# Kernel optimization log

Hardware: AMD Instinct MI355X
Metric: run time of the kernel (lower is better)

The kernel has to match this reference:

```python
import jax, jax.numpy as jnp
import numpy as np
from jax import lax

B, S, H = 2, 2048, 768
FF = 1536
E = 8
TOP_K = 2


def setup_inputs() -> dict:
    key = jax.random.key(0)
    k1, k2, k3, k4 = jax.random.split(key, 4)
    hidden_states = jax.random.normal(k1, (B, S, H), dtype=jnp.float32)
    # torch init: weight.normal_() for experts; nn.Linear default init for gate (approx normal here is fine for a numerics baseline)
    gate_w = jax.random.normal(k2, (E, H), dtype=jnp.float32) * 0.02
    w_fc = jax.random.normal(k3, (E, FF, H), dtype=jnp.float32) * 0.02
    w_proj = jax.random.normal(k4, (E, H, FF), dtype=jnp.float32) * 0.02
    return {"hidden_states": hidden_states, "gate_w": gate_w, "w_fc": w_fc, "w_proj": w_proj}


def reference(hidden_states, gate_w, w_fc, w_proj):
    b, s, h = hidden_states.shape
    x = hidden_states.reshape(-1, h)                      # [T, H]
    # --- top-k gating (logits in float32, as in the torch code) ---
    logits = (x @ gate_w.T).astype(jnp.float32)           # [T, E]
    top_logits, top_idx = lax.top_k(logits, TOP_K)        # [T, K]
    gates = jax.nn.softmax(top_logits, axis=1).astype(x.dtype)  # [T, K]
    # combined per-token/per-expert gate: g[t,e] = sum_k gates[t,k]*[idx[t,k]==e]
    onehot = jax.nn.one_hot(top_idx, E, dtype=x.dtype)    # [T, K, E]
    g = jnp.einsum('tk,tke->te', gates, onehot)           # [T, E]
    # --- experts: gather + per-expert GEMM + gated scatter-add combine ---
    # Equivalent math: tokens with zero gate for expert e contribute nothing,
    # so compute each expert on all tokens and weight by g[:, e].
    out = jnp.zeros_like(x)
    for e in range(E):  # fixed small loop over experts (structurally distinct weights)
        hmid = jax.nn.gelu(x @ w_fc[e].T, approximate=False)   # [T, FF] (torch gelu = erf form)
        out = out + g[:, e:e + 1] * (hmid @ w_proj[e].T)       # [T, H]
    out = out.reshape(b, s, h)
    return out, logits
```

## Files before the change

kernel.cpp:

```cpp
#include <hip/hip_runtime.h>
#include <hip/hip_bf16.h>
#include <math.h>
#include <stdint.h>

#define TOKENS 4096
#define HDIM   768
#define FFDIM  1536
#define NEXP   8

typedef __attribute__((ext_vector_type(8))) short bf16x8;
typedef __attribute__((ext_vector_type(4))) float f32x4;

__device__ __forceinline__ unsigned short f2bf(float f) {
    union { float f; uint32_t u; } c; c.f = f;
    uint32_t u = c.u;
    uint32_t r = (u + 0x7FFFu + ((u >> 16) & 1u)) >> 16;
    return (unsigned short)r;
}

__device__ __forceinline__ void gload_lds16(const void* g, void* l) {
    __builtin_amdgcn_global_load_lds(
        (const __attribute__((address_space(1))) void*)g,
        (__attribute__((address_space(3))) void*)l, 16, 0, 0);
}

__global__ void zero_init(float* __restrict__ outp, int n) {
    int i = blockIdx.x * blockDim.x + threadIdx.x;
    int stride = gridDim.x * blockDim.x;
    for (int j = i; j < n; j += stride) outp[j] = 0.f;
}

__global__ void cast_bf16(const float* __restrict__ src,
                          unsigned short* __restrict__ dst, int n4) {
    int stride = gridDim.x * blockDim.x;
    for (int i = blockIdx.x * blockDim.x + threadIdx.x; i < n4; i += stride) {
        float4 v = ((const float4*)src)[i];
        ushort4 o;
        o.x = f2bf(v.x); o.y = f2bf(v.y); o.z = f2bf(v.z); o.w = f2bf(v.w);
        ((ushort4*)dst)[i] = o;
    }
}

__global__ __launch_bounds__(256) void gating(
    const float* __restrict__ x, const float* __restrict__ gw,
    float* __restrict__ logits,
    int* __restrict__ tok_e, float* __restrict__ tok_g)
{
    int t = blockIdx.x * 4 + (threadIdx.x >> 6);
    int lane = threadIdx.x & 63;
    const float4* xt = (const float4*)(x + (size_t)t * HDIM);
    const float4* gw4 = (const float4*)gw;
    float acc[NEXP];
#pragma unroll
    for (int e = 0; e < NEXP; e++) acc[e] = 0.f;
#pragma unroll
    for (int it = 0; it < 3; it++) {
        int i = lane + it * 64;
        float4 xv = xt[i];
#pragma unroll
        for (int e = 0; e < NEXP; e++) {
            float4 wv = gw4[e * 192 + i];
            acc[e] += xv.x * wv.x + xv.y * wv.y + xv.z * wv.z + xv.w * wv.w;
        }
    }
#pragma unroll
    for (int e = 0; e < NEXP; e++) {
#pragma unroll
        for (int off = 32; off > 0; off >>= 1)
            acc[e] += __shfl_xor(acc[e], off);
    }
    if (lane == 0) {
        float4 l0 = make_float4(acc[0], acc[1], acc[2], acc[3]);
        float4 l1 = make_float4(acc[4], acc[5], acc[6], acc[7]);
        float4* lp = (float4*)(logits + (size_t)t * NEXP);
        lp[0] = l0; lp[1] = l1;
        int i0 = 0; float v0 = acc[0];
#pragma unroll
        for (int e = 1; e < NEXP; e++) if (acc[e] > v0) { v0 = acc[e]; i0 = e; }
        int i1 = -1; float v1 = -3.4e38f;
#pragma unroll
        for (int e = 0; e < NEXP; e++) if (e != i0 && acc[e] > v1) { v1 = acc[e]; i1 = e; }
        float g0 = 1.f / (1.f + expf(v1 - v0));
        tok_e[t * 2] = i0; tok_e[t * 2 + 1] = i1;
        tok_g[t * 2] = g0; tok_g[t * 2 + 1] = 1.f - g0;
    }
}

__global__ __launch_bounds__(1024) void build_lists(
    const int* __restrict__ tok_e, const float* __restrict__ tok_g,
    int* __restrict__ counts, int* __restrict__ entries,
    float* __restrict__ gates)
{
    __shared__ unsigned long long slo[1024], shi[1024];
    int tid = threadIdx.x;
    int eL[8]; float gL[8];
    int4 ea = ((const int4*)tok_e)[tid * 2];
    int4 eb = ((const int4*)tok_e)[tid * 2 + 1];
    float4 ga = ((const float4*)tok_g)[tid * 2];
    float4 gb = ((const float4*)tok_g)[tid * 2 + 1];
    eL[0] = ea.x; eL[1] = ea.y; eL[2] = ea.z; eL[3] = ea.w;
    eL[4] = eb.x; eL[5] = eb.y; eL[6] = eb.z; eL[7] = eb.w;
    gL[0] = ga.x; gL[1] = ga.y; gL[2] = ga.z; gL[3] = ga.w;
    gL[4] = gb.x; gL[5] = gb.y; gL[6] = gb.z; gL[7] = gb.w;

    unsigned long long clo = 0, chi = 0;
#pragma unroll
    for (int j = 0; j < 8; j++) {
        int e = eL[j];
        unsigned long long one = 1ull << ((e & 3) * 16);
        if (e < 4) clo += one; else chi += one;
    }
    slo[tid] = clo; shi[tid] = chi;
    __syncthreads();
    for (int s = 1; s < 1024; s <<= 1) {
        unsigned long long vlo = 0, vhi = 0;
        if (tid >= s) { vlo = slo[tid - s]; vhi = shi[tid - s]; }
        __syncthreads();
        slo[tid] += vlo; shi[tid] += vhi;
        __syncthreads();
    }
    unsigned long long rlo = slo[tid] - clo;
    unsigned long long rhi = shi[tid] - chi;
    if (tid == 0) {
        unsigned long long tlo = slo[1023], thi = shi[1023];
#pragma unroll
        for (int e = 0; e < 4; e++) {
            counts[e]     = (int)((tlo >> (e * 16)) & 0xFFFF);
            counts[e + 4] = (int)((thi >> (e * 16)) & 0xFFFF);
        }
    }
#pragma unroll
    for (int j = 0; j < 8; j++) {
        int e = eL[j];
        int sh = (e & 3) * 16;
        unsigned long long one = 1ull << sh;
        int slot;
        if (e < 4) { slot = (int)((rlo >> sh) & 0xFFFF); rlo += one; }
        else       { slot = (int)((rhi >> sh) & 0xFFFF); rhi += one; }
        entries[e * TOKENS + slot] = tid * 8 + j;
        gates[e * TOKENS + slot]   = gL[j];
    }
}

template<int KD, int ND, bool IS_FC>
__global__ __launch_bounds__(256) void moe_gemm(
    const unsigned short* __restrict__ Asrc,
    const unsigned short* __restrict__ Bsrc,
    const int* __restrict__ counts,
    const int* __restrict__ entries,
    const float* __restrict__ gates,
    unsigned short* __restrict__ hmid,
    float* __restrict__ outp)
{
    int e = blockIdx.z;
    int n_e = counts[e];
    int rowTile = blockIdx.y;
    if (rowTile * 64 >= n_e) return;
    int n0 = blockIdx.x * 64;

    __shared__ __align__(16) unsigned short sA[64 * 32];
    __shared__ __align__(16) unsigned short sB[64 * 32];

    int tid = threadIdx.x;
    int w = tid >> 6;
    int l = tid & 63;

    const int* lst = entries + e * TOKENS;

    int rL   = (w << 4) + (l >> 2);
    int p    = l & 3;
    int sseg = p ^ ((rL >> 1) & 3);

    int lrow = rowTile * 64 + rL;
    int idx  = lrow < n_e ? lrow : n_e - 1;
    int ent  = lst[idx];
    int arow = IS_FC ? (ent >> 1) : ent;

    const unsigned short* Ab = Asrc + (size_t)arow * KD + sseg * 8;
    const unsigned short* Bb = Bsrc + (size_t)e * ND * KD + (size_t)(n0 + rL) * KD + sseg * 8;
    unsigned short* sAw = sA + w * 512;
    unsigned short* sBw = sB + w * 512;

    int lo = l & 15;
    int q  = l >> 4;
    int pa = q ^ ((lo >> 1) & 3);
    int aOff     = w * 512 + lo * 32 + pa * 8;
    int bOffBase = lo * 32 + pa * 8;

    f32x4 acc[4];
#pragma unroll
    for (int i = 0; i < 4; i++) acc[i] = (f32x4){0.f, 0.f, 0.f, 0.f};

    for (int k0 = 0; k0 < KD; k0 += 32) {
        gload_lds16(Ab + k0, sAw);
        gload_lds16(Bb + k0, sBw);
        __syncthreads();
        bf16x8 va = *(const bf16x8*)(sA + aOff);
#pragma unroll
        for (int nt = 0; nt < 4; nt++) {
            bf16x8 vb = *(const bf16x8*)(sB + nt * 512 + bOffBase);
            acc[nt] = __builtin_amdgcn_mfma_f32_16x16x32_bf16(va, vb, acc[nt], 0, 0, 0);
        }
        __syncthreads();
    }

#pragma unroll
    for (int r = 0; r < 4; r++) {
        int orow = rowTile * 64 + (w << 4) + q * 4 + r;
        if (orow < n_e) {
            int oent = lst[orow];
            if (IS_FC) {
                size_t rowid = (size_t)oent;
#pragma unroll
                for (int nt = 0; nt < 4; nt++) {
                    float v = acc[nt][r];
                    v = 0.5f * v * (1.f + erff(v * 0.70710678118654752f));
                    hmid[rowid * FFDIM + n0 + nt * 16 + lo] = f2bf(v);
                }
            } else {
                int token = oent >> 1;
                float g = gates[e * TOKENS + orow];
#pragma unroll
                for (int nt = 0; nt < 4; nt++) {
                    atomicAdd(&outp[(size_t)token * HDIM + n0 + nt * 16 + lo],
                              acc[nt][r] * g);
                }
            }
        }
    }
}

extern "C" void kernel_launch(void* const* d_in, const int* in_sizes, int n_in,
                              void* d_out, int out_size, void* d_ws, size_t ws_size,
                              hipStream_t stream) {
    const float* x     = (const float*)d_in[0];
    const float* gw    = (const float*)d_in[1];
    const float* wfc   = (const float*)d_in[2];
    const float* wproj = (const float*)d_in[3];
    float* outp   = (float*)d_out;
    float* logits = outp + (size_t)TOKENS * HDIM;

    char* ws = (char*)d_ws;
    int*   counts  = (int*)ws;
    int*   entries = (int*)(ws + 256);
    float* gates   = (float*)(ws + 256 + NEXP * TOKENS * 4);
    size_t off = 256 + 2ull * NEXP * TOKENS * 4;
    int*   tok_e   = (int*)(ws + off);   off += (size_t)TOKENS * 2 * 4;
    float* tok_g   = (float*)(ws + off); off += (size_t)TOKENS * 2 * 4;
    unsigned short* x_bf   = (unsigned short*)(ws + off); off += (size_t)TOKENS * HDIM * 2;
    unsigned short* wfc_bf = (unsigned short*)(ws + off); off += (size_t)NEXP * FFDIM * HDIM * 2;
    unsigned short* wpj_bf = (unsigned short*)(ws + off); off += (size_t)NEXP * HDIM * FFDIM * 2;
    unsigned short* hmid   = (unsigned short*)(ws + off);

    zero_init<<<2048, 256, 0, stream>>>(outp, TOKENS * HDIM);
    cast_bf16<<<1536, 256, 0, stream>>>(x, x_bf, TOKENS * HDIM / 4);
    cast_bf16<<<2048, 256, 0, stream>>>(wfc, wfc_bf, NEXP * FFDIM * HDIM / 4);
    cast_bf16<<<2048, 256, 0, stream>>>(wproj, wpj_bf, NEXP * HDIM * FFDIM / 4);
    gating<<<TOKENS / 4, 256, 0, stream>>>(x, gw, logits, tok_e, tok_g);
    build_lists<<<1, 1024, 0, stream>>>(tok_e, tok_g, counts, entries, gates);
    moe_gemm<HDIM, FFDIM, true ><<<dim3(FFDIM / 64, 64, NEXP), 256, 0, stream>>>(
        x_bf, wfc_bf, counts, entries, gates, hmid, outp);
    moe_gemm<FFDIM, HDIM, false><<<dim3(HDIM / 64, 64, NEXP), 256, 0, stream>>>(
        hmid, wpj_bf, counts, entries, gates, hmid, outp);
}
```

Measured before the change: 264.8 us.

## Enlarge MoE GEMM tiles to 128x128, compact hmid layout, fuse x cast into gating

The MoE GEMM tile grows from 64x64 to 128x128, with each wave computing a 64x64 sub-tile of 4x4 MFMAs, so each loaded operand is reused more and LDS and global traffic per FLOP drops. hmid is now stored in expert-sorted compact rows (base offset plus slot) instead of indexed by entry, so the second GEMM reads its A rows contiguously. The separate x-to-bf16 cast kernel is folded into the gating kernel, removing one launch and one read of x. The trade-off is more accumulator registers per thread, lower occupancy, and fewer blocks in flight.

```diff
diff --git a/kernel.cpp b/kernel.cpp
--- a/kernel.cpp
+++ b/kernel.cpp
@@ -44,12 +44,14 @@
 __global__ __launch_bounds__(256) void gating(
     const float* __restrict__ x, const float* __restrict__ gw,
     float* __restrict__ logits,
-    int* __restrict__ tok_e, float* __restrict__ tok_g)
+    int* __restrict__ tok_e, float* __restrict__ tok_g,
+    unsigned short* __restrict__ x_bf)
 {
     int t = blockIdx.x * 4 + (threadIdx.x >> 6);
     int lane = threadIdx.x & 63;
     const float4* xt = (const float4*)(x + (size_t)t * HDIM);
     const float4* gw4 = (const float4*)gw;
+    ushort4* xbt = (ushort4*)(x_bf + (size_t)t * HDIM);
     float acc[NEXP];
 #pragma unroll
     for (int e = 0; e < NEXP; e++) acc[e] = 0.f;
@@ -57,6 +59,9 @@
     for (int it = 0; it < 3; it++) {
         int i = lane + it * 64;
         float4 xv = xt[i];
+        ushort4 o;
+        o.x = f2bf(xv.x); o.y = f2bf(xv.y); o.z = f2bf(xv.z); o.w = f2bf(xv.w);
+        xbt[i] = o;
 #pragma unroll
         for (int e = 0; e < NEXP; e++) {
             float4 wv = gw4[e * 192 + i];
@@ -88,8 +93,8 @@
 
 __global__ __launch_bounds__(1024) void build_lists(
     const int* __restrict__ tok_e, const float* __restrict__ tok_g,
-    int* __restrict__ counts, int* __restrict__ entries,
-    float* __restrict__ gates)
+    int* __restrict__ counts, int* __restrict__ bases,
+    int* __restrict__ entries, float* __restrict__ gates)
 {
     __shared__ unsigned long long slo[1024], shi[1024];
     int tid = threadIdx.x;
@@ -123,11 +128,15 @@
     unsigned long long rhi = shi[tid] - chi;
     if (tid == 0) {
         unsigned long long tlo = slo[1023], thi = shi[1023];
+        int c[8];
 #pragma unroll
         for (int e = 0; e < 4; e++) {
-            counts[e]     = (int)((tlo >> (e * 16)) & 0xFFFF);
-            counts[e + 4] = (int)((thi >> (e * 16)) & 0xFFFF);
+            c[e]     = (int)((tlo >> (e * 16)) & 0xFFFF);
+            c[e + 4] = (int)((thi >> (e * 16)) & 0xFFFF);
         }
+        int b = 0;
+#pragma unroll
+        for (int e = 0; e < NEXP; e++) { counts[e] = c[e]; bases[e] = b; b += c[e]; }
     }
 #pragma unroll
     for (int j = 0; j < 8; j++) {
@@ -147,6 +156,7 @@
     const unsigned short* __restrict__ Asrc,
     const unsigned short* __restrict__ Bsrc,
     const int* __restrict__ counts,
+    const int* __restrict__ bases,
     const int* __restrict__ entries,
     const float* __restrict__ gates,
     unsigned short* __restrict__ hmid,
@@ -155,75 +165,101 @@
     int e = blockIdx.z;
     int n_e = counts[e];
     int rowTile = blockIdx.y;
-    if (rowTile * 64 >= n_e) return;
-    int n0 = blockIdx.x * 64;
-
-    __shared__ __align__(16) unsigned short sA[64 * 32];
-    __shared__ __align__(16) unsigned short sB[64 * 32];
+    if (rowTile * 128 >= n_e) return;
+    int ebase = bases[e];
+    int n0 = blockIdx.x * 128;
+
+    __shared__ __align__(16) unsigned short sA[128 * 32];
+    __shared__ __align__(16) unsigned short sB[128 * 32];
 
     int tid = threadIdx.x;
     int w = tid >> 6;
     int l = tid & 63;
-
     const int* lst = entries + e * TOKENS;
 
-    int rL   = (w << 4) + (l >> 2);
-    int p    = l & 3;
-    int sseg = p ^ ((rL >> 1) & 3);
-
-    int lrow = rowTile * 64 + rL;
-    int idx  = lrow < n_e ? lrow : n_e - 1;
-    int ent  = lst[idx];
-    int arow = IS_FC ? (ent >> 1) : ent;
-
-    const unsigned short* Ab = Asrc + (size_t)arow * KD + sseg * 8;
-    const unsigned short* Bb = Bsrc + (size_t)e * ND * KD + (size_t)(n0 + rL) * KD + sseg * 8;
-    unsigned short* sAw = sA + w * 512;
-    unsigned short* sBw = sB + w * 512;
+    int r0 = w * 32 + (l >> 2);
+    int r1 = r0 + 16;
+    int p  = l & 3;
+    int ss0 = p ^ ((r0 >> 1) & 3);
+    int ss1 = p ^ ((r1 >> 1) & 3);
+
+    int lr0 = rowTile * 128 + r0;
+    int lr1 = rowTile * 128 + r1;
+    int id0 = lr0 < n_e ? lr0 : n_e - 1;
+    int id1 = lr1 < n_e ? lr1 : n_e - 1;
+    size_t arow0, arow1;
+    if (IS_FC) { arow0 = (size_t)(lst[id0] >> 1); arow1 = (size_t)(lst[id1] >> 1); }
+    else       { arow0 = (size_t)(ebase + id0);   arow1 = (size_t)(ebase + id1);   }
+
+    const unsigned short* Ag0 = Asrc + arow0 * KD + ss0 * 8;
+    const unsigned short* Ag1 = Asrc + arow1 * KD + ss1 * 8;
+    const unsigned short* Bg0 = Bsrc + ((size_t)e * ND + n0 + r0) * KD + ss0 * 8;
+    const unsigned short* Bg1 = Bsrc + ((size_t)e * ND + n0 + r1) * KD + ss1 * 8;
+    unsigned short* sA0 = sA + (2 * w)     * 512;
+    unsigned short* sA1 = sA + (2 * w + 1) * 512;
+    unsigned short* sB0 = sB + (2 * w)     * 512;
+    unsigned short* sB1 = sB + (2 * w + 1) * 512;
 
     int lo = l & 15;
     int q  = l >> 4;
-    int pa = q ^ ((lo >> 1) & 3);
-    int aOff     = w * 512 + lo * 32 + pa * 8;
-    int bOffBase = lo * 32 + pa * 8;
-
-    f32x4 acc[4];
-#pragma unroll
-    for (int i = 0; i < 4; i++) acc[i] = (f32x4){0.f, 0.f, 0.f, 0.f};
+    int wr = w >> 1, wc = w & 1;
+    int aOff[4], bOff[4];
+#pragma unroll
+    for (int i = 0; i < 4; i++) {
+        int m = wr * 64 + i * 16 + lo;
+        aOff[i] = m * 32 + (q ^ ((m >> 1) & 3)) * 8;
+        int n = wc * 64 + i * 16 + lo;
+        bOff[i] = n * 32 + (q ^ ((n >> 1) & 3)) * 8;
+    }
+
+    f32x4 acc[4][4];
+#pragma unroll
+    for (int i = 0; i < 4; i++)
+#pragma unroll
+        for (int j = 0; j < 4; j++) acc[i][j] = (f32x4){0.f, 0.f, 0.f, 0.f};
 
     for (int k0 = 0; k0 < KD; k0 += 32) {
-        gload_lds16(Ab + k0, sAw);
-        gload_lds16(Bb + k0, sBw);
+        gload_lds16(Ag0 + k0, sA0);
+        gload_lds16(Ag1 + k0, sA1);
+        gload_lds16(Bg0 + k0, sB0);
+        gload_lds16(Bg1 + k0, sB1);
         __syncthreads();
-        bf16x8 va = *(const bf16x8*)(sA + aOff);
-#pragma unroll
-        for (int nt = 0; nt < 4; nt++) {
-            bf16x8 vb = *(const bf16x8*)(sB + nt * 512 + bOffBase);
-            acc[nt] = __builtin_amdgcn_mfma_f32_16x16x32_bf16(va, vb, acc[nt], 0, 0, 0);
-        }
+        bf16x8 a[4], b[4];
+#pragma unroll
+        for (int i = 0; i < 4; i++) a[i] = *(const bf16x8*)(sA + aOff[i]);
+#pragma unroll
+        for (int j = 0; j < 4; j++) b[j] = *(const bf16x8*)(sB + bOff[j]);
+#pragma unroll
+        for (int i = 0; i < 4; i++)
+#pragma unroll
+            for (int j = 0; j < 4; j++)
+                acc[i][j] = __builtin_amdgcn_mfma_f32_16x16x32_bf16(a[i], b[j], acc[i][j], 0, 0, 0);
         __syncthreads();
     }
 
 #pragma unroll
-    for (int r = 0; r < 4; r++) {
-        int orow = rowTile * 64 + (w << 4) + q * 4 + r;
-        if (orow < n_e) {
-            int oent = lst[orow];
-            if (IS_FC) {
-                size_t rowid = (size_t)oent;
-#pragma unroll
-                for (int nt = 0; nt < 4; nt++) {
-                    float v = acc[nt][r];
-                    v = 0.5f * v * (1.f + erff(v * 0.70710678118654752f));
-                    hmid[rowid * FFDIM + n0 + nt * 16 + lo] = f2bf(v);
-                }
-            } else {
-                int token = oent >> 1;
-                float g = gates[e * TOKENS + orow];
-#pragma unroll
-                for (int nt = 0; nt < 4; nt++) {
-                    atomicAdd(&outp[(size_t)token * HDIM + n0 + nt * 16 + lo],
-                              acc[nt][r] * g);
+    for (int i = 0; i < 4; i++) {
+        int rowB = rowTile * 128 + wr * 64 + i * 16 + q * 4;
+#pragma unroll
+        for (int rr = 0; rr < 4; rr++) {
+            int orow = rowB + rr;
+            if (orow < n_e) {
+                if (IS_FC) {
+                    size_t hrow = (size_t)(ebase + orow);
+#pragma unroll
+                    for (int j = 0; j < 4; j++) {
+                        float v = acc[i][j][rr];
+                        v = 0.5f * v * (1.f + erff(v * 0.70710678118654752f));
+                        hmid[hrow * ND + n0 + wc * 64 + j * 16 + lo] = f2bf(v);
+                    }
+                } else {
+                    int token = lst[orow] >> 1;
+                    float g = gates[e * TOKENS + orow];
+#pragma unroll
+                    for (int j = 0; j < 4; j++) {
+                        atomicAdd(&outp[(size_t)token * ND + n0 + wc * 64 + j * 16 + lo],
+                                  acc[i][j][rr] * g);
+                    }
                 }
             }
         }
@@ -242,6 +278,7 @@
 
     char* ws = (char*)d_ws;
     int*   counts  = (int*)ws;
+    int*   bases   = (int*)(ws + 64);
     int*   entries = (int*)(ws + 256);
     float* gates   = (float*)(ws + 256 + NEXP * TOKENS * 4);
     size_t off = 256 + 2ull * NEXP * TOKENS * 4;
@@ -253,13 +290,12 @@
     unsigned short* hmid   = (unsigned short*)(ws + off);
 
     zero_init<<<2048, 256, 0, stream>>>(outp, TOKENS * HDIM);
-    cast_bf16<<<1536, 256, 0, stream>>>(x, x_bf, TOKENS * HDIM / 4);
     cast_bf16<<<2048, 256, 0, stream>>>(wfc, wfc_bf, NEXP * FFDIM * HDIM / 4);
     cast_bf16<<<2048, 256, 0, stream>>>(wproj, wpj_bf, NEXP * HDIM * FFDIM / 4);
-    gating<<<TOKENS / 4, 256, 0, stream>>>(x, gw, logits, tok_e, tok_g);
-    build_lists<<<1, 1024, 0, stream>>>(tok_e, tok_g, counts, entries, gates);
-    moe_gemm<HDIM, FFDIM, true ><<<dim3(FFDIM / 64, 64, NEXP), 256, 0, stream>>>(
-        x_bf, wfc_bf, counts, entries, gates, hmid, outp);
-    moe_gemm<FFDIM, HDIM, false><<<dim3(HDIM / 64, 64, NEXP), 256, 0, stream>>>(
-        hmid, wpj_bf, counts, entries, gates, hmid, outp);
-}
+    gating<<<TOKENS / 4, 256, 0, stream>>>(x, gw, logits, tok_e, tok_g, x_bf);
+    build_lists<<<1, 1024, 0, stream>>>(tok_e, tok_g, counts, bases, entries, gates);
+    moe_gemm<HDIM, FFDIM, true ><<<dim3(FFDIM / 128, TOKENS / 128, NEXP), 256, 0, stream>>>(
+        x_bf, wfc_bf, counts, bases, entries, gates, hmid, outp);
+    moe_gemm<FFDIM, HDIM, false><<<dim3(HDIM / 128, TOKENS / 128, NEXP), 256, 0, stream>>>(
+        hmid, wpj_bf, counts, bases, entries, gates, hmid, outp);
+}
```

After: 250.8 us. -5.3%, faster.
